# Kernel optimization log

Measured on AMD Instinct MI355X. Metric: run time of the kernel, lower is better.

## Reference

```python
import jax, jax.numpy as jnp
import numpy as np

N = 8192
IN_F = 512
OUT_F = 64
NEG_SLOPE = 0.01  # nn.LeakyReLU default
MASK_VAL = -1e9


def setup_inputs() -> dict:
    key = jax.random.key(0)
    k_h, k_adj, k_W, k_a = jax.random.split(key, 4)
    h = jax.random.normal(k_h, (N, IN_F), dtype=jnp.float32)
    adjacency = jax.random.randint(k_adj, (N, N), 0, 2, dtype=jnp.int32)
    # xavier_uniform bounds
    bW = float(np.sqrt(6.0 / (IN_F + OUT_F)))
    ba = float(np.sqrt(6.0 / (2 * OUT_F + 1)))
    W = jax.random.uniform(k_W, (IN_F, OUT_F), minval=-bW, maxval=bW, dtype=jnp.float32)
    a = jax.random.uniform(k_a, (2 * OUT_F, 1), minval=-ba, maxval=ba, dtype=jnp.float32)
    return {"h": h, "adjacency": adjacency, "W": W, "a": a}


def reference(h, adjacency, W, a):
    WH = h @ W                                  # [N, out_f]
    wh1 = WH @ a[:OUT_F, :]                     # [N, 1]
    wh2 = WH @ a[OUT_F:, :]                     # [N, 1]
    e = jax.nn.leaky_relu(wh1 + wh2.T, negative_slope=NEG_SLOPE)  # [N, N]
    attnt = jnp.where(adjacency > 0, e, jnp.float32(MASK_VAL))
    attnt = jax.nn.softmax(attnt, axis=1)       # row-wise softmax
    hfirst = attnt @ WH                         # [N, out_f]
    return jax.nn.elu(hfirst)
```

## Files before the change

kernel.cpp:

```cpp
#include <hip/hip_runtime.h>
#include <hip/hip_bf16.h>

#define N 8192
#define IN_F 512
#define OUT_F 64
#define S_SPLIT 16
#define JT (N / S_SPLIT)
#define NB (N / 8)
#define LDP 520

typedef __attribute__((ext_vector_type(8))) short short8;
typedef __attribute__((ext_vector_type(4))) float floatx4;
typedef __attribute__((ext_vector_type(4))) int intx4;

__device__ inline short f2bf(float x) {
    __hip_bfloat16 b = __float2bfloat16(x);
    return __builtin_bit_cast(short, b);
}

__global__ __launch_bounds__(256) void k_pack(const int* __restrict__ adj,
                                              unsigned* __restrict__ mask) {
    int wv = (blockIdx.x * 256 + threadIdx.x) >> 6;
    int lane = threadIdx.x & 63;
    const int* p = adj + (size_t)wv * 512 + lane;
    unsigned long long m0 = __ballot(p[0]   > 0);
    unsigned long long m1 = __ballot(p[64]  > 0);
    unsigned long long m2 = __ballot(p[128] > 0);
    unsigned long long m3 = __ballot(p[192] > 0);
    unsigned long long m4 = __ballot(p[256] > 0);
    unsigned long long m5 = __ballot(p[320] > 0);
    unsigned long long m6 = __ballot(p[384] > 0);
    unsigned long long m7 = __ballot(p[448] > 0);
    if (lane < 16) {
        unsigned long long s0 = (lane & 2) ? m1 : m0;
        unsigned long long s1 = (lane & 2) ? m3 : m2;
        unsigned long long s2 = (lane & 2) ? m5 : m4;
        unsigned long long s3 = (lane & 2) ? m7 : m6;
        unsigned long long t0 = (lane & 4) ? s1 : s0;
        unsigned long long t1 = (lane & 4) ? s3 : s2;
        unsigned long long u  = (lane & 8) ? t1 : t0;
        unsigned dw = (lane & 1) ? (unsigned)(u >> 32) : (unsigned)u;
        mask[wv * 16 + lane] = dw;
    }
}

__global__ void k_wt(const float* __restrict__ W, short* __restrict__ WT) {
    int idx = blockIdx.x * 256 + threadIdx.x;
    int k = idx >> 6, f = idx & 63;
    WT[f * IN_F + k] = f2bf(W[k * OUT_F + f]);
}

__global__ __launch_bounds__(64) void k_wh(const float* __restrict__ h,
                                           const short* __restrict__ WT,
                                           const float* __restrict__ a,
                                           short* __restrict__ WHbT,
                                           float* __restrict__ wh1,
                                           float* __restrict__ wh2) {
    __shared__ float tile[OUT_F][17];
    int lane = threadIdx.x;
    int n = lane & 15, q = lane >> 4;
    int i0 = blockIdx.x * 16;
    int rowA = i0 + n;
    const float* hp = h + (size_t)rowA * IN_F + q * 8;
    floatx4 acc[4] = {};
    for (int k0 = 0; k0 < IN_F; k0 += 32) {
        floatx4 h0 = *(const floatx4*)(hp + k0);
        floatx4 h1 = *(const floatx4*)(hp + k0 + 4);
        short8 af;
#pragma unroll
        for (int j = 0; j < 4; j++) { af[j] = f2bf(h0[j]); af[j + 4] = f2bf(h1[j]); }
#pragma unroll
        for (int b = 0; b < 4; b++) {
            short8 bf_ = *(const short8*)(WT + (b * 16 + n) * IN_F + k0 + q * 8);
            acc[b] = __builtin_amdgcn_mfma_f32_16x16x32_bf16(af, bf_, acc[b], 0, 0, 0);
        }
    }
#pragma unroll
    for (int b = 0; b < 4; b++)
#pragma unroll
        for (int r = 0; r < 4; r++)
            tile[b * 16 + n][q * 4 + r] = acc[b][r];
    float a1v[4], a2v[4];
#pragma unroll
    for (int b = 0; b < 4; b++) { a1v[b] = a[b * 16 + n]; a2v[b] = a[OUT_F + b * 16 + n]; }
#pragma unroll
    for (int r = 0; r < 4; r++) {
        float s1 = 0.f, s2 = 0.f;
#pragma unroll
        for (int b = 0; b < 4; b++) { s1 += acc[b][r] * a1v[b]; s2 += acc[b][r] * a2v[b]; }
#pragma unroll
        for (int m = 1; m <= 8; m <<= 1) {
            s1 += __shfl_xor(s1, m, 64);
            s2 += __shfl_xor(s2, m, 64);
        }
        if (n == 0) {
            wh1[i0 + q * 4 + r] = s1;
            wh2[i0 + q * 4 + r] = s2;
        }
    }
    __syncthreads();
    const float* tc = tile[lane];
    short8 s0, s1v;
#pragma unroll
    for (int k = 0; k < 8; k++) { s0[k] = f2bf(tc[k]); s1v[k] = f2bf(tc[k + 8]); }
    *(short8*)(WHbT + (size_t)lane * N + i0) = s0;
    *(short8*)(WHbT + (size_t)lane * N + i0 + 8) = s1v;
}

__global__ __launch_bounds__(256, 2) void k_attn(const unsigned char* __restrict__ mask,
                                                 const short* __restrict__ WHbT,
                                                 const float* __restrict__ wh1,
                                                 const float* __restrict__ wh2,
                                                 float* __restrict__ num_part,
                                                 float* __restrict__ den_part) {
    __shared__ short ldsb[OUT_F * LDP];
    int tid = threadIdx.x;
    int w = tid >> 6;
    int lane = tid & 63;
    int n = lane & 15, q = lane >> 4;
    int split = blockIdx.y;
    int j0 = split * JT;
    int i0 = blockIdx.x * 256 + w * 64;

#pragma unroll
    for (int l = 0; l < 16; l++) {
        int idx = l * 256 + tid;
        int f = idx >> 6, c16 = idx & 63;
        short8 v = *(const short8*)(WHbT + (size_t)f * N + j0 + c16 * 8);
        *(short8*)(ldsb + f * LDP + c16 * 8) = v;
    }
    __syncthreads();

    float wh1f[4];
#pragma unroll
    for (int rf = 0; rf < 4; rf++) wh1f[rf] = wh1[i0 + rf * 16 + n];

    floatx4 acc[4][4] = {};
    float dsum[4] = {0.f, 0.f, 0.f, 0.f};
    const float* w2p = wh2 + j0 + q * 8;
    const short* lp = ldsb + q * 8;
    int qs = q * 8;

    intx4 mcur[4], mnxt[4];
#pragma unroll
    for (int rf = 0; rf < 4; rf++)
        mcur[rf] = *(const intx4*)(mask + (size_t)(i0 + rf * 16 + n) * NB + split * 64);

    for (int g = 0; g < 4; g++) {
        if (g < 3) {
#pragma unroll
            for (int rf = 0; rf < 4; rf++)
                mnxt[rf] = *(const intx4*)(mask + (size_t)(i0 + rf * 16 + n) * NB
                                           + split * 64 + (g + 1) * 16);
        }
#pragma unroll
        for (int d = 0; d < 4; d++) {
            int s = g * 4 + d;
            floatx4 w20 = *(const floatx4*)(w2p + s * 32);
            floatx4 w21 = *(const floatx4*)(w2p + s * 32 + 4);
            short8 bfr[4];
#pragma unroll
            for (int b = 0; b < 4; b++)
                bfr[b] = *(const short8*)(lp + (b * 16 + n) * LDP + s * 32);
#pragma unroll
            for (int rf = 0; rf < 4; rf++) {
                unsigned md = (unsigned)mcur[rf][d];
                float p[8];
#pragma unroll
                for (int jj = 0; jj < 8; jj++) {
                    float e = wh1f[rf] + ((jj < 4) ? w20[jj] : w21[jj - 4]);
                    float el = fmaxf(e, 0.01f * e);
                    float pv = __expf(el);
                    pv = ((md >> (qs + jj)) & 1u) ? pv : 0.f;
                    p[jj] = pv;
                    dsum[rf] += pv;
                }
                short8 af;
#pragma unroll
                for (int jj = 0; jj < 8; jj++) af[jj] = f2bf(p[jj]);
#pragma unroll
                for (int b = 0; b < 4; b++)
                    acc[rf][b] = __builtin_amdgcn_mfma_f32_16x16x32_bf16(af, bfr[b], acc[rf][b], 0, 0, 0);
            }
        }
#pragma unroll
        for (int rf = 0; rf < 4; rf++) mcur[rf] = mnxt[rf];
    }

#pragma unroll
    for (int rf = 0; rf < 4; rf++) {
        float d = dsum[rf];
        d += __shfl_xor(d, 16, 64);
        d += __shfl_xor(d, 32, 64);
        if (q == 0) den_part[(size_t)split * N + i0 + rf * 16 + n] = d;
    }

    float* np_ = num_part + (size_t)split * N * OUT_F;
#pragma unroll
    for (int rf = 0; rf < 4; rf++)
#pragma unroll
        for (int b = 0; b < 4; b++)
#pragma unroll
            for (int r = 0; r < 4; r++)
                np_[(size_t)(i0 + rf * 16 + q * 4 + r) * OUT_F + b * 16 + n] = acc[rf][b][r];
}

__global__ void k_final(const float* __restrict__ num_part,
                        const float* __restrict__ den_part,
                        float* __restrict__ out) {
    int idx = blockIdx.x * 256 + threadIdx.x;
    int row = idx >> 6;
    float s = 0.f, d = 0.f;
#pragma unroll
    for (int sp = 0; sp < S_SPLIT; sp++) {
        s += num_part[(size_t)sp * N * OUT_F + idx];
        d += den_part[sp * N + row];
    }
    float x = s / d;
    out[idx] = (x > 0.f) ? x : (__expf(x) - 1.f);
}

extern "C" void kernel_launch(void* const* d_in, const int* in_sizes, int n_in,
                              void* d_out, int out_size, void* d_ws, size_t ws_size,
                              hipStream_t stream) {
    const float* h = (const float*)d_in[0];
    const int* adj = (const int*)d_in[1];
    const float* W = (const float*)d_in[2];
    const float* a = (const float*)d_in[3];
    float* out = (float*)d_out;

    char* ws = (char*)d_ws;
    short* WHbT     = (short*)(ws);
    short* WT       = (short*)(ws + (size_t)(1 << 20));
    float* wh1      = (float*)(ws + (size_t)(1 << 20) + (64 << 10));
    float* wh2      = wh1 + N;
    unsigned* maskb = (unsigned*)(ws + (size_t)(2 << 20));
    float* num_p    = (float*)(ws + (size_t)(16 << 20));
    float* den_p    = (float*)(ws + (size_t)(48 << 20));

    k_pack<<<dim3((N / 32) * (N / 256) * 4), dim3(256), 0, stream>>>(adj, maskb);
    k_wt<<<dim3(128), dim3(256), 0, stream>>>(W, WT);
    k_wh<<<dim3(N / 16), dim3(64), 0, stream>>>(h, WT, a, WHbT, wh1, wh2);
    k_attn<<<dim3(N / 256, S_SPLIT), dim3(256), 0, stream>>>((const unsigned char*)maskb,
                                                             WHbT, wh1, wh2, num_p, den_p);
    k_final<<<dim3((N * OUT_F) / 256), dim3(256), 0, stream>>>(num_p, den_p, out);
}
```

Before: 411.1 us.

## Fuse adjacency bit-packing into attention kernel and read WH directly from global

Drops the separate mask-packing kernel. Each wave of the attention kernel now ballots its own 64 adjacency rows over its column slice into a small LDS bitmask. The WH^T tile is no longer staged in shared memory; B fragments are loaded straight from global memory (L2/cache). This removes one launch and the round trip of the packed mask through global memory. The cost is that adjacency loads now serialize ahead of the MFMA loop inside each block, B-fragment global loads have higher latency, and the occupancy hint of 2 is removed.

```diff
diff --git a/kernel.cpp b/kernel.cpp
--- a/kernel.cpp
+++ b/kernel.cpp
@@ -6,8 +6,7 @@
 #define OUT_F 64
 #define S_SPLIT 16
 #define JT (N / S_SPLIT)
-#define NB (N / 8)
-#define LDP 520
+#define MP 20
 
 typedef __attribute__((ext_vector_type(8))) short short8;
 typedef __attribute__((ext_vector_type(4))) float floatx4;
@@ -16,32 +15,6 @@
 __device__ inline short f2bf(float x) {
     __hip_bfloat16 b = __float2bfloat16(x);
     return __builtin_bit_cast(short, b);
-}
-
-__global__ __launch_bounds__(256) void k_pack(const int* __restrict__ adj,
-                                              unsigned* __restrict__ mask) {
-    int wv = (blockIdx.x * 256 + threadIdx.x) >> 6;
-    int lane = threadIdx.x & 63;
-    const int* p = adj + (size_t)wv * 512 + lane;
-    unsigned long long m0 = __ballot(p[0]   > 0);
-    unsigned long long m1 = __ballot(p[64]  > 0);
-    unsigned long long m2 = __ballot(p[128] > 0);
-    unsigned long long m3 = __ballot(p[192] > 0);
-    unsigned long long m4 = __ballot(p[256] > 0);
-    unsigned long long m5 = __ballot(p[320] > 0);
-    unsigned long long m6 = __ballot(p[384] > 0);
-    unsigned long long m7 = __ballot(p[448] > 0);
-    if (lane < 16) {
-        unsigned long long s0 = (lane & 2) ? m1 : m0;
-        unsigned long long s1 = (lane & 2) ? m3 : m2;
-        unsigned long long s2 = (lane & 2) ? m5 : m4;
-        unsigned long long s3 = (lane & 2) ? m7 : m6;
-        unsigned long long t0 = (lane & 4) ? s1 : s0;
-        unsigned long long t1 = (lane & 4) ? s3 : s2;
-        unsigned long long u  = (lane & 8) ? t1 : t0;
-        unsigned dw = (lane & 1) ? (unsigned)(u >> 32) : (unsigned)u;
-        mask[wv * 16 + lane] = dw;
-    }
 }
 
 __global__ void k_wt(const float* __restrict__ W, short* __restrict__ WT) {
@@ -107,13 +80,13 @@
     *(short8*)(WHbT + (size_t)lane * N + i0 + 8) = s1v;
 }
 
-__global__ __launch_bounds__(256, 2) void k_attn(const unsigned char* __restrict__ mask,
-                                                 const short* __restrict__ WHbT,
-                                                 const float* __restrict__ wh1,
-                                                 const float* __restrict__ wh2,
-                                                 float* __restrict__ num_part,
-                                                 float* __restrict__ den_part) {
-    __shared__ short ldsb[OUT_F * LDP];
+__global__ __launch_bounds__(256) void k_attn(const int* __restrict__ adj,
+                                              const short* __restrict__ WHbT,
+                                              const float* __restrict__ wh1,
+                                              const float* __restrict__ wh2,
+                                              float* __restrict__ num_part,
+                                              float* __restrict__ den_part) {
+    __shared__ unsigned ldsm[4 * 64 * MP];
     int tid = threadIdx.x;
     int w = tid >> 6;
     int lane = tid & 63;
@@ -122,14 +95,32 @@
     int j0 = split * JT;
     int i0 = blockIdx.x * 256 + w * 64;
 
-#pragma unroll
-    for (int l = 0; l < 16; l++) {
-        int idx = l * 256 + tid;
-        int f = idx >> 6, c16 = idx & 63;
-        short8 v = *(const short8*)(WHbT + (size_t)f * N + j0 + c16 * 8);
-        *(short8*)(ldsb + f * LDP + c16 * 8) = v;
-    }
-    __syncthreads();
+    unsigned* mym = ldsm + w * 64 * MP;
+    for (int rr = 0; rr < 64; rr += 2) {
+#pragma unroll
+        for (int u = 0; u < 2; u++) {
+            const int* p = adj + (size_t)(i0 + rr + u) * N + j0 + lane;
+            unsigned long long m0 = __ballot(p[0]   > 0);
+            unsigned long long m1 = __ballot(p[64]  > 0);
+            unsigned long long m2 = __ballot(p[128] > 0);
+            unsigned long long m3 = __ballot(p[192] > 0);
+            unsigned long long m4 = __ballot(p[256] > 0);
+            unsigned long long m5 = __ballot(p[320] > 0);
+            unsigned long long m6 = __ballot(p[384] > 0);
+            unsigned long long m7 = __ballot(p[448] > 0);
+            if (lane < 16) {
+                unsigned long long s0 = (lane & 2) ? m1 : m0;
+                unsigned long long s1 = (lane & 2) ? m3 : m2;
+                unsigned long long s2 = (lane & 2) ? m5 : m4;
+                unsigned long long s3 = (lane & 2) ? m7 : m6;
+                unsigned long long t0 = (lane & 4) ? s1 : s0;
+                unsigned long long t1 = (lane & 4) ? s3 : s2;
+                unsigned long long uq = (lane & 8) ? t1 : t0;
+                unsigned dw = (lane & 1) ? (unsigned)(uq >> 32) : (unsigned)uq;
+                mym[(rr + u) * MP + lane] = dw;
+            }
+        }
+    }
 
     float wh1f[4];
 #pragma unroll
@@ -138,21 +129,14 @@
     floatx4 acc[4][4] = {};
     float dsum[4] = {0.f, 0.f, 0.f, 0.f};
     const float* w2p = wh2 + j0 + q * 8;
-    const short* lp = ldsb + q * 8;
+    const short* bp0 = WHbT + (size_t)n * N + j0 + q * 8;
     int qs = q * 8;
 
-    intx4 mcur[4], mnxt[4];
-#pragma unroll
-    for (int rf = 0; rf < 4; rf++)
-        mcur[rf] = *(const intx4*)(mask + (size_t)(i0 + rf * 16 + n) * NB + split * 64);
-
     for (int g = 0; g < 4; g++) {
-        if (g < 3) {
-#pragma unroll
-            for (int rf = 0; rf < 4; rf++)
-                mnxt[rf] = *(const intx4*)(mask + (size_t)(i0 + rf * 16 + n) * NB
-                                           + split * 64 + (g + 1) * 16);
-        }
+        intx4 mrf[4];
+#pragma unroll
+        for (int rf = 0; rf < 4; rf++)
+            mrf[rf] = *(const intx4*)(mym + (rf * 16 + n) * MP + g * 4);
 #pragma unroll
         for (int d = 0; d < 4; d++) {
             int s = g * 4 + d;
@@ -161,10 +145,10 @@
             short8 bfr[4];
 #pragma unroll
             for (int b = 0; b < 4; b++)
-                bfr[b] = *(const short8*)(lp + (b * 16 + n) * LDP + s * 32);
+                bfr[b] = *(const short8*)(bp0 + (size_t)b * 16 * N + s * 32);
 #pragma unroll
             for (int rf = 0; rf < 4; rf++) {
-                unsigned md = (unsigned)mcur[rf][d];
+                unsigned md = (unsigned)mrf[rf][d];
                 float p[8];
 #pragma unroll
                 for (int jj = 0; jj < 8; jj++) {
@@ -183,8 +167,6 @@
                     acc[rf][b] = __builtin_amdgcn_mfma_f32_16x16x32_bf16(af, bfr[b], acc[rf][b], 0, 0, 0);
             }
         }
-#pragma unroll
-        for (int rf = 0; rf < 4; rf++) mcur[rf] = mnxt[rf];
     }
 
 #pragma unroll
@@ -230,18 +212,16 @@
     float* out = (float*)d_out;
 
     char* ws = (char*)d_ws;
-    short* WHbT     = (short*)(ws);
-    short* WT       = (short*)(ws + (size_t)(1 << 20));
-    float* wh1      = (float*)(ws + (size_t)(1 << 20) + (64 << 10));
-    float* wh2      = wh1 + N;
-    unsigned* maskb = (unsigned*)(ws + (size_t)(2 << 20));
-    float* num_p    = (float*)(ws + (size_t)(16 << 20));
-    float* den_p    = (float*)(ws + (size_t)(48 << 20));
-
-    k_pack<<<dim3((N / 32) * (N / 256) * 4), dim3(256), 0, stream>>>(adj, maskb);
+    short* WHbT  = (short*)(ws);
+    short* WT    = (short*)(ws + (size_t)(1 << 20));
+    float* wh1   = (float*)(ws + (size_t)(1 << 20) + (64 << 10));
+    float* wh2   = wh1 + N;
+    float* num_p = (float*)(ws + (size_t)(16 << 20));
+    float* den_p = (float*)(ws + (size_t)(48 << 20));
+
     k_wt<<<dim3(128), dim3(256), 0, stream>>>(W, WT);
     k_wh<<<dim3(N / 16), dim3(64), 0, stream>>>(h, WT, a, WHbT, wh1, wh2);
-    k_attn<<<dim3(N / 256, S_SPLIT), dim3(256), 0, stream>>>((const unsigned char*)maskb,
-                                                             WHbT, wh1, wh2, num_p, den_p);
+    k_attn<<<dim3(N / 256, S_SPLIT), dim3(256), 0, stream>>>(adj, WHbT, wh1, wh2,
+                                                             num_p, den_p);
     k_final<<<dim3((N * OUT_F) / 256), dim3(256), 0, stream>>>(num_p, den_p, out);
 }
```

Measured after the change: 433.1 us. 1.05x slower.
